# Kernel tuning notes

Hardware: AMD Instinct MI355X
Metric: run time of the kernel (lower is better)

## Reference

```python
import jax, jax.numpy as jnp
import numpy as np

N = 20000      # nodes
E = 320000     # edges (before self-loops)
G = 64         # graphs in batch
IN = 128       # in_channels
HID = 64       # hidden_dim
NEG_SLOPE = 0.2


def setup_inputs() -> dict:
    key = jax.random.key(0)
    ks = jax.random.split(key, 20)
    def glorot(k, shape):
        fan = shape[0] + shape[-1]
        return jax.random.normal(k, shape, jnp.float32) * np.sqrt(2.0 / fan)
    inp = {
        'x': jax.random.normal(ks[0], (N, IN), jnp.float32),
        'edge_index': jax.random.randint(ks[1], (2, E), 0, N, jnp.int32),
        'batch': jnp.sort(jax.random.randint(ks[2], (N,), 0, G, jnp.int32)),
        # GAT layer 1: heads=4, out=64, concat=False
        'W1': glorot(ks[3], (IN, 4 * HID)),
        'as1': glorot(ks[4], (4, HID)),
        'ad1': glorot(ks[5], (4, HID)),
        'b1': jnp.zeros((HID,), jnp.float32),
        # GAT layer 2: heads=2, out=32, concat=False
        'W2': glorot(ks[6], (HID, 2 * (HID // 2))),
        'as2': glorot(ks[7], (2, HID // 2)),
        'ad2': glorot(ks[8], (2, HID // 2)),
        'b2': jnp.zeros((HID // 2,), jnp.float32),
        # continue head: 32->16->1
        'cW1': glorot(ks[9], (HID // 2, HID // 4)), 'cb1': jnp.zeros((HID // 4,), jnp.float32),
        'cW2': glorot(ks[10], (HID // 4, 1)), 'cb2': jnp.zeros((1,), jnp.float32),
        # halt head: 32->16->1
        'hW1': glorot(ks[11], (HID // 2, HID // 4)), 'hb1': jnp.zeros((HID // 4,), jnp.float32),
        'hW2': glorot(ks[12], (HID // 4, 1)), 'hb2': jnp.zeros((1,), jnp.float32),
    }
    return inp


def gat_layer(x, src, dst, W, att_src, att_dst, bias, heads, out_ch):
    # x: [N, Fin] -> h: [N, H, C]
    n = x.shape[0]
    h = (x @ W).reshape(n, heads, out_ch)
    a_src = jnp.einsum('nhc,hc->nh', h, att_src)   # [N, H]
    a_dst = jnp.einsum('nhc,hc->nh', h, att_dst)   # [N, H]
    e = jax.nn.leaky_relu(a_src[src] + a_dst[dst], NEG_SLOPE)   # [E', H]
    # segment softmax over incoming edges of each dst node
    m = jax.ops.segment_max(e, dst, num_segments=n)             # [N, H]
    ee = jnp.exp(e - m[dst])
    denom = jax.ops.segment_sum(ee, dst, num_segments=n)        # [N, H]
    alpha = ee / (denom[dst] + 1e-16)                           # [E', H]
    msg = h[src] * alpha[:, :, None]                            # [E', H, C]
    out = jax.ops.segment_sum(msg, dst, num_segments=n)         # [N, H, C]
    return out.mean(axis=1) + bias                              # concat=False -> head mean


def reference(x, edge_index, batch, W1, as1, ad1, b1, W2, as2, ad2, b2,
              cW1, cb1, cW2, cb2, hW1, hb1, hW2, hb2):
    n = x.shape[0]
    loop = jnp.arange(n, dtype=edge_index.dtype)
    src = jnp.concatenate([edge_index[0], loop])   # add self-loops (PyG default)
    dst = jnp.concatenate([edge_index[1], loop])

    h1 = jax.nn.relu(gat_layer(x, src, dst, W1, as1, ad1, b1, 4, HID))
    h2 = jax.nn.relu(gat_layer(h1, src, dst, W2, as2, ad2, b2, 2, HID // 2))

    # global mean pool per graph
    sums = jax.ops.segment_sum(h2, batch, num_segments=G)                 # [G, 32]
    cnt = jax.ops.segment_sum(jnp.ones((n,), h2.dtype), batch, num_segments=G)
    emb = sums / jnp.maximum(cnt, 1.0)[:, None]                           # [G, 32]

    cont = jax.nn.sigmoid(jax.nn.relu(emb @ cW1 + cb1) @ cW2 + cb2)       # [G, 1]
    halt = jax.nn.sigmoid(jax.nn.relu(emb @ hW1 + hb1) @ hW2 + hb2)       # [G, 1]
    return (halt, cont)
```

## Files before the change

### kernel.cpp

```cpp
#include <hip/hip_runtime.h>
#include <hip/hip_fp16.h>


#define G_GRAPHS 64

using half8   = __attribute__((ext_vector_type(8))) _Float16;
using half4v  = __attribute__((ext_vector_type(4))) _Float16;
using floatx4 = __attribute__((ext_vector_type(4))) float;
using floatx2 = __attribute__((ext_vector_type(2))) float;

__global__ __launch_bounds__(256) void init_deg_ell(
        int4* __restrict__ deg4, int* __restrict__ col_ell, int N)
{
    int i = blockIdx.x * 256 + threadIdx.x;
    int n4 = N * 4;
    if (i < n4) {
        deg4[i] = ((i & 3) == 0) ? int4{1, 0, 0, 0} : int4{0, 0, 0, 0};
        if ((i & 3) == 0) {
            int n = i >> 2;
            col_ell[(size_t)n * 64] = n;
        }
    }
}

__global__ __launch_bounds__(256) void ell_gemm1(
        const int* __restrict__ ei, int* __restrict__ deg16,
        int* __restrict__ col_ell, int E0, int mb,
        const float* __restrict__ A, const float* __restrict__ B,
        unsigned char* __restrict__ C8, const float* __restrict__ att_s,
        const float* __restrict__ att_d, float* __restrict__ a_s,
        float* __restrict__ a_d, int M)
{
    __shared__ _Float16 As[64][136];
    __shared__ _Float16 Bt[64][136];

    if ((int)blockIdx.x >= mb) {
        int idx4 = ((int)blockIdx.x - mb) * 1024 + threadIdx.x * 4;
        if (idx4 + 3 < E0) {
            int4 s4 = *reinterpret_cast<const int4*>(&ei[idx4]);
            int4 d4 = *reinterpret_cast<const int4*>(&ei[E0 + idx4]);
            int sl0 = atomicAdd(&deg16[d4.x << 4], 1);
            int sl1 = atomicAdd(&deg16[d4.y << 4], 1);
            int sl2 = atomicAdd(&deg16[d4.z << 4], 1);
            int sl3 = atomicAdd(&deg16[d4.w << 4], 1);
            if (sl0 < 64) col_ell[(size_t)d4.x * 64 + sl0] = s4.x;
            if (sl1 < 64) col_ell[(size_t)d4.y * 64 + sl1] = s4.y;
            if (sl2 < 64) col_ell[(size_t)d4.z * 64 + sl2] = s4.z;
            if (sl3 < 64) col_ell[(size_t)d4.w * 64 + sl3] = s4.w;
        } else {
            for (int j = 0; j < 4; j++) {
                int idx = idx4 + j;
                if (idx < E0) {
                    int src = ei[idx];
                    int dst = ei[E0 + idx];
                    int slot = atomicAdd(&deg16[dst << 4], 1);
                    if (slot < 64)
                        col_ell[(size_t)dst * 64 + slot] = src;
                }
            }
        }
        return;
    }

    const int tid  = threadIdx.x;
    const int row0 = blockIdx.x * 64;
    const int wid  = tid >> 6;
    const int lane = tid & 63;
    const int r    = lane & 15;
    const int quad = lane >> 4;
    const int rw0  = wid * 16;

    const int arow = tid >> 2;
    const int akc  = (tid & 3) * 32;
    const int agr  = row0 + arow;

    #pragma unroll
    for (int i = 0; i < 4; i++) {
        half8 v = {};
        if (agr < M) {
            const float* p = &A[(size_t)agr * 128 + akc + i * 8];
            float4 f0 = *reinterpret_cast<const float4*>(p);
            float4 f1 = *reinterpret_cast<const float4*>(p + 4);
            v[0] = (_Float16)f0.x; v[1] = (_Float16)f0.y;
            v[2] = (_Float16)f0.z; v[3] = (_Float16)f0.w;
            v[4] = (_Float16)f1.x; v[5] = (_Float16)f1.y;
            v[6] = (_Float16)f1.z; v[7] = (_Float16)f1.w;
        }
        *reinterpret_cast<half8*>(&As[arow][akc + i * 8]) = v;
    }

    for (int by = 0; by < 4; by++) {
        __syncthreads();

        #pragma unroll
        for (int i = 0; i < 8; i++) {
            int id = tid + 256 * i;
            int k  = id >> 4;
            int n4 = (id & 15) * 4;
            float4 f = *reinterpret_cast<const float4*>(
                &B[(size_t)k * 256 + by * 64 + n4]);
            Bt[n4 + 0][k] = (_Float16)f.x;
            Bt[n4 + 1][k] = (_Float16)f.y;
            Bt[n4 + 2][k] = (_Float16)f.z;
            Bt[n4 + 3][k] = (_Float16)f.w;
        }
        __syncthreads();

        floatx4 acc[4] = {};
        #pragma unroll
        for (int s = 0; s < 4; s++) {
            half8 af = *reinterpret_cast<const half8*>(&As[rw0 + r][s * 32 + quad * 8]);
            #pragma unroll
            for (int nt = 0; nt < 4; nt++) {
                half8 bf = *reinterpret_cast<const half8*>(&Bt[nt * 16 + r][s * 32 + quad * 8]);
                acc[nt] = __builtin_amdgcn_mfma_f32_16x16x32_f16(af, bf, acc[nt], 0, 0, 0);
            }
        }

        float ps[4], pd[4];
        #pragma unroll
        for (int reg = 0; reg < 4; reg++) { ps[reg] = 0.f; pd[reg] = 0.f; }
        #pragma unroll
        for (int nt = 0; nt < 4; nt++) {
            int cl = nt * 16 + r;
            float ws = att_s[by * 64 + cl];
            float wd = att_d[by * 64 + cl];
            #pragma unroll
            for (int reg = 0; reg < 4; reg++) {
                ps[reg] += acc[nt][reg] * ws;
                pd[reg] += acc[nt][reg] * wd;
            }
        }
        #pragma unroll
        for (int off = 1; off < 16; off <<= 1)
            #pragma unroll
            for (int reg = 0; reg < 4; reg++) {
                ps[reg] += __shfl_xor(ps[reg], off);
                pd[reg] += __shfl_xor(pd[reg], off);
            }
        if (r == 0) {
            #pragma unroll
            for (int reg = 0; reg < 4; reg++) {
                int gr = row0 + rw0 + quad * 4 + reg;
                if (gr < M) {
                    a_s[gr * 4 + by] = ps[reg];
                    a_d[gr * 4 + by] = pd[reg];
                }
            }
        }

        __syncthreads();
        unsigned char (*lds8)[80] = reinterpret_cast<unsigned char(*)[80]>(&Bt[0][0]);
        #pragma unroll
        for (int nt = 0; nt < 4; nt++) {
            #pragma unroll
            for (int reg = 0; reg < 4; reg++) {
                int wv = __builtin_amdgcn_cvt_pk_fp8_f32(
                    acc[nt][reg], acc[nt][reg], 0, false);
                lds8[rw0 + quad * 4 + reg][nt * 16 + r] = (unsigned char)(wv & 0xFF);
            }
        }
        __syncthreads();
        {
            int row = tid >> 2;
            int c16 = (tid & 3) * 16;
            int gr  = row0 + row;
            if (gr < M) {
                int4 v = *reinterpret_cast<const int4*>(&lds8[row][c16]);
                *reinterpret_cast<int4*>(&C8[(size_t)gr * 256 + by * 64 + c16]) = v;
            }
        }
    }
}

__global__ __launch_bounds__(256) void gemm2_kernel(
        const _Float16* __restrict__ A, const float* __restrict__ B,
        unsigned char* __restrict__ C8, const float* __restrict__ att_s,
        const float* __restrict__ att_d, float* __restrict__ a_s,
        float* __restrict__ a_d, int M)
{
    __shared__ _Float16 As[64][72];
    __shared__ _Float16 Bt[64][72];

    const int tid  = threadIdx.x;
    const int row0 = blockIdx.x * 64;

    {
        int row = tid >> 2;
        int kc  = (tid & 3) * 16;
        int gr  = row0 + row;
        #pragma unroll
        for (int i = 0; i < 2; i++) {
            half8 v = {};
            if (gr < M)
                v = *reinterpret_cast<const half8*>(&A[(size_t)gr * 64 + kc + i * 8]);
            *reinterpret_cast<half8*>(&As[row][kc + i * 8]) = v;
        }
    }
    {
        #pragma unroll
        for (int i = 0; i < 4; i++) {
            int id = tid + 256 * i;
            int k  = id >> 4;
            int n4 = (id & 15) * 4;
            float4 f = *reinterpret_cast<const float4*>(&B[(size_t)k * 64 + n4]);
            Bt[n4 + 0][k] = (_Float16)f.x;
            Bt[n4 + 1][k] = (_Float16)f.y;
            Bt[n4 + 2][k] = (_Float16)f.z;
            Bt[n4 + 3][k] = (_Float16)f.w;
        }
    }
    __syncthreads();

    const int wid  = tid >> 6;
    const int lane = tid & 63;
    const int r    = lane & 15;
    const int quad = lane >> 4;
    const int rw0  = wid * 16;

    floatx4 acc[4] = {};
    #pragma unroll
    for (int s = 0; s < 2; s++) {
        half8 af = *reinterpret_cast<const half8*>(&As[rw0 + r][s * 32 + quad * 8]);
        #pragma unroll
        for (int nt = 0; nt < 4; nt++) {
            half8 bf = *reinterpret_cast<const half8*>(&Bt[nt * 16 + r][s * 32 + quad * 8]);
            acc[nt] = __builtin_amdgcn_mfma_f32_16x16x32_f16(af, bf, acc[nt], 0, 0, 0);
        }
    }

    float ps[2][4], pd[2][4];
    #pragma unroll
    for (int hl = 0; hl < 2; hl++)
        #pragma unroll
        for (int reg = 0; reg < 4; reg++) { ps[hl][reg] = 0.f; pd[hl][reg] = 0.f; }
    #pragma unroll
    for (int nt = 0; nt < 4; nt++) {
        int hl = nt >> 1;
        int cl = (nt & 1) * 16 + r;
        float ws = att_s[hl * 32 + cl];
        float wd = att_d[hl * 32 + cl];
        #pragma unroll
        for (int reg = 0; reg < 4; reg++) {
            ps[hl][reg] += acc[nt][reg] * ws;
            pd[hl][reg] += acc[nt][reg] * wd;
        }
    }
    #pragma unroll
    for (int off = 1; off < 16; off <<= 1)
        #pragma unroll
        for (int hl = 0; hl < 2; hl++)
            #pragma unroll
            for (int reg = 0; reg < 4; reg++) {
                ps[hl][reg] += __shfl_xor(ps[hl][reg], off);
                pd[hl][reg] += __shfl_xor(pd[hl][reg], off);
            }
    if (r == 0) {
        #pragma unroll
        for (int reg = 0; reg < 4; reg++) {
            int gr = row0 + rw0 + quad * 4 + reg;
            if (gr < M) {
                #pragma unroll
                for (int hl = 0; hl < 2; hl++) {
                    a_s[gr * 2 + hl] = ps[hl][reg];
                    a_d[gr * 2 + hl] = pd[hl][reg];
                }
            }
        }
    }

    __syncthreads();
    unsigned char (*lds8)[80] = reinterpret_cast<unsigned char(*)[80]>(&As[0][0]);
    #pragma unroll
    for (int nt = 0; nt < 4; nt++) {
        #pragma unroll
        for (int reg = 0; reg < 4; reg++) {
            int wv = __builtin_amdgcn_cvt_pk_fp8_f32(
                acc[nt][reg], acc[nt][reg], 0, false);
            lds8[rw0 + quad * 4 + reg][nt * 16 + r] = (unsigned char)(wv & 0xFF);
        }
    }
    __syncthreads();
    {
        int row = tid >> 2;
        int c16 = (tid & 3) * 16;
        int gr  = row0 + row;
        if (gr < M) {
            int4 v = *reinterpret_cast<const int4*>(&lds8[row][c16]);
            *reinterpret_cast<int4*>(&C8[(size_t)gr * 64 + c16]) = v;
        }
    }
}

__device__ inline void facc4_h(float* a, float2 raw, float p) {
    __half2 h0 = *reinterpret_cast<__half2*>(&raw.x);
    __half2 h1 = *reinterpret_cast<__half2*>(&raw.y);
    float2 f0 = __half22float2(h0), f1 = __half22float2(h1);
    a[0] += p * f0.x; a[1] += p * f0.y; a[2] += p * f1.x; a[3] += p * f1.y;
}
__device__ inline void facc4_8(float* a, unsigned int w, float p) {
    floatx2 lo = __builtin_amdgcn_cvt_pk_f32_fp8((int)w, false);
    floatx2 hi = __builtin_amdgcn_cvt_pk_f32_fp8((int)w, true);
    a[0] += p * lo[0]; a[1] += p * lo[1]; a[2] += p * hi[0]; a[3] += p * hi[1];
}
__device__ inline void facc8_8(float* a, uint2 w, float p) {
    facc4_8(a,     w.x, p);
    facc4_8(a + 4, w.y, p);
}
__device__ inline float fp8_dec1(unsigned char b) {
    floatx2 lo = __builtin_amdgcn_cvt_pk_f32_fp8((int)(unsigned int)b, false);
    return lo[0];
}

template<int H, int C, bool OUT_HALF, bool FEAT_FP8>
__device__ void gat_general(
        int d, int lo, int degc, const int* __restrict__ colidx,
        const void* __restrict__ hfeat_v, const float* __restrict__ a_s,
        const float* __restrict__ a_d, const float* __restrict__ bias,
        void* __restrict__ out_v, int N, float* p_wave)
{
    if (d >= N) return;
    constexpr int FV = (H * C) / 64;
    const int lane = threadIdx.x & 63;
    const int hi = lo + degc;
    const __half* hfeat = (const __half*)hfeat_v;
    const unsigned char* ffeat = (const unsigned char*)hfeat_v;
    const int h_lane = (lane * FV) / C;

    float adp[H];
    #pragma unroll
    for (int h = 0; h < H; h++) adp[h] = a_d[d * H + h];
    float lh[H];
    #pragma unroll
    for (int h = 0; h < H; h++) lh[h] = 0.f;
    float acc[FV];
    #pragma unroll
    for (int v = 0; v < FV; v++) acc[v] = 0.f;

    float mh[H];
    #pragma unroll
    for (int h = 0; h < H; h++) mh[h] = -3.0e38f;
    for (int i = lo + lane; i < hi; i += 64) {
        int s = colidx[i];
        #pragma unroll
        for (int h = 0; h < H; h++) {
            float v = a_s[s * H + h] + adp[h];
            v = (v > 0.f) ? v : 0.2f * v;
            mh[h] = fmaxf(mh[h], v);
        }
    }
    #pragma unroll
    for (int off = 1; off < 64; off <<= 1)
        #pragma unroll
        for (int h = 0; h < H; h++)
            mh[h] = fmaxf(mh[h], __shfl_xor(mh[h], off));

    for (int base = lo; base < hi; base += 64) {
        int i = base + lane;
        int s = 0;
        if (i < hi) {
            s = colidx[i];
            #pragma unroll
            for (int h = 0; h < H; h++) {
                float v = a_s[s * H + h] + adp[h];
                v = (v > 0.f) ? v : 0.2f * v;
                float p = __expf(v - mh[h]);
                lh[h] += p;
                p_wave[(i - base) * H + h] = p;
            }
        }
        int cnt = min(64, hi - base);
        for (int j = 0; j < cnt; j++) {
            int s_j = __shfl(s, j);
            float pj = p_wave[j * H + h_lane];
            if constexpr (FV == 4 && FEAT_FP8) {
                unsigned int raw = *reinterpret_cast<const unsigned int*>(
                    ffeat + (size_t)s_j * (H * C) + lane * 4);
                facc4_8(acc, raw, pj);
            } else if constexpr (FV == 4) {
                float2 raw = *reinterpret_cast<const float2*>(
                    hfeat + (size_t)s_j * (H * C) + lane * 4);
                facc4_h(acc, raw, pj);
            } else if constexpr (FEAT_FP8) {
                acc[0] += pj * fp8_dec1(ffeat[(size_t)s_j * (H * C) + lane]);
            } else {
                acc[0] += pj * __half2float(hfeat[(size_t)s_j * (H * C) + lane]);
            }
        }
    }
    #pragma unroll
    for (int off = 1; off < 64; off <<= 1)
        #pragma unroll
        for (int h = 0; h < H; h++)
            lh[h] += __shfl_xor(lh[h], off);

    float lsel = lh[0];
    #pragma unroll
    for (int h = 1; h < H; h++) if (h_lane == h) lsel = lh[h];
    const float inv = 1.0f / (lsel + 1e-16f);

    if constexpr (FV == 4) {
        float vx = acc[0] * inv, vy = acc[1] * inv,
              vz = acc[2] * inv, vw = acc[3] * inv;
        vx += __shfl_xor(vx, 16); vy += __shfl_xor(vy, 16);
        vz += __shfl_xor(vz, 16); vw += __shfl_xor(vw, 16);
        vx += __shfl_xor(vx, 32); vy += __shfl_xor(vy, 32);
        vz += __shfl_xor(vz, 32); vw += __shfl_xor(vw, 32);
        if (lane < 16) {
            float4 bv = *reinterpret_cast<const float4*>(&bias[lane * 4]);
            float ox = fmaxf(0.25f * vx + bv.x, 0.f);
            float oy = fmaxf(0.25f * vy + bv.y, 0.f);
            float oz = fmaxf(0.25f * vz + bv.z, 0.f);
            float ow = fmaxf(0.25f * vw + bv.w, 0.f);
            if constexpr (OUT_HALF) {
                half4v hv = { (_Float16)ox, (_Float16)oy, (_Float16)oz, (_Float16)ow };
                *reinterpret_cast<half4v*>((_Float16*)out_v + (size_t)d * C + lane * 4) = hv;
            } else {
                float4 o = make_float4(ox, oy, oz, ow);
                *reinterpret_cast<float4*>((float*)out_v + (size_t)d * C + lane * 4) = o;
            }
        }
    } else {
        float v = acc[0] * inv;
        v += __shfl_xor(v, 32);
        if (lane < 32) {
            float o = fmaxf(0.5f * v + bias[lane], 0.f);
            if constexpr (OUT_HALF)
                ((_Float16*)out_v)[(size_t)d * C + lane] = (_Float16)o;
            else
                ((float*)out_v)[(size_t)d * C + lane] = o;
        }
    }
}

template<int H, int C, bool OUT_HALF, bool FEAT_FP8>
__global__ __launch_bounds__(256) void gat_dst(
        const int* __restrict__ degv, const int* __restrict__ col_ell,
        const void* __restrict__ hfeat_v, const float* __restrict__ a_s,
        const float* __restrict__ a_d, const float* __restrict__ bias,
        void* __restrict__ out_v, int N)
{
    const int wid  = threadIdx.x >> 6;
    const int lane = threadIdx.x & 63;
    const int nw   = lane >> 5;
    const int l32  = lane & 31;

    __shared__ float p_sh[4][64 * H];

    const int d  = blockIdx.x * 8 + wid * 2 + nw;
    const bool nodeok = (d < N);
    const int lo = d * 64;

    int degc = 0;
    if (nodeok) degc = min(degv[d << 4], 64);
    const int degA = __shfl(degc, 0);
    const int degB = __shfl(degc, 32);
    const bool fast = (degA <= 32) && (degB <= 32);

    if (fast) {
        const __half* hfeat = (const __half*)hfeat_v;
        const unsigned char* ffeat = (const unsigned char*)hfeat_v;

        float adp[H];
        #pragma unroll
        for (int h = 0; h < H; h++) adp[h] = nodeok ? a_d[d * H + h] : 0.f;

        int s = 0;
        float lh[H];
        #pragma unroll
        for (int h = 0; h < H; h++) lh[h] = 0.f;
        const bool valid = nodeok && (l32 < degc);
        if (valid) {
            s = col_ell[lo + l32];
            if constexpr (H == 4) {
                float4 av = *reinterpret_cast<const float4*>(&a_s[s * 4]);
                float ev[4] = {av.x + adp[0], av.y + adp[1],
                               av.z + adp[2], av.w + adp[3]};
                #pragma unroll
                for (int h = 0; h < 4; h++) {
                    float e = (ev[h] > 0.f) ? ev[h] : 0.2f * ev[h];
                    float p = __expf(e);
                    lh[h] = p;
                    p_sh[wid][nw * 32 * H + l32 * H + h] = p;
                }
            } else {
                float2 av = *reinterpret_cast<const float2*>(&a_s[s * 2]);
                float ev[2] = {av.x + adp[0], av.y + adp[1]};
                #pragma unroll
                for (int h = 0; h < 2; h++) {
                    float e = (ev[h] > 0.f) ? ev[h] : 0.2f * ev[h];
                    float p = __expf(e);
                    lh[h] = p;
                    p_sh[wid][nw * 32 * H + l32 * H + h] = p;
                }
            }
        }
        #pragma unroll
        for (int off = 1; off < 32; off <<= 1)
            #pragma unroll
            for (int h = 0; h < H; h++)
                lh[h] += __shfl_xor(lh[h], off);

        const int sbase = nw * 32;

        if constexpr (H == 4) {
            const int hl = l32 >> 3;
            float a0[8] = {}, a1[8] = {};
            int j = 0;
            for (; j + 8 <= degc; j += 8) {
                uint2 raw[8]; float pw[8];
                #pragma unroll
                for (int u = 0; u < 8; u++) {
                    int sj = __shfl(s, sbase + j + u);
                    pw[u]  = p_sh[wid][nw * 128 + (j + u) * 4 + hl];
                    raw[u] = *reinterpret_cast<const uint2*>(
                        ffeat + (size_t)sj * 256 + l32 * 8);
                }
                #pragma unroll
                for (int u = 0; u < 8; u++)
                    facc8_8((u & 1) ? a1 : a0, raw[u], pw[u]);
            }
            for (; j < degc; j++) {
                int sj = __shfl(s, sbase + j);
                float pw = p_sh[wid][nw * 128 + j * 4 + hl];
                uint2 raw = *reinterpret_cast<const uint2*>(
                    ffeat + (size_t)sj * 256 + l32 * 8);
                facc8_8(a0, raw, pw);
            }
            #pragma unroll
            for (int k = 0; k < 8; k++) a0[k] += a1[k];

            float lsel = lh[0];
            #pragma unroll
            for (int h = 1; h < 4; h++) if (hl == h) lsel = lh[h];
            float inv = 1.0f / (lsel + 1e-16f);
            #pragma unroll
            for (int k = 0; k < 8; k++) {
                float v = a0[k] * inv;
                v += __shfl_xor(v, 8);
                v += __shfl_xor(v, 16);
                a0[k] = v;
            }
            if (nodeok && l32 < 8) {
                float4 b0 = *reinterpret_cast<const float4*>(&bias[l32 * 8]);
                float4 b1 = *reinterpret_cast<const float4*>(&bias[l32 * 8 + 4]);
                float bb[8] = {b0.x, b0.y, b0.z, b0.w, b1.x, b1.y, b1.z, b1.w};
                half8 hv;
                #pragma unroll
                for (int k = 0; k < 8; k++)
                    hv[k] = (_Float16)fmaxf(0.25f * a0[k] + bb[k], 0.f);
                *reinterpret_cast<half8*>((_Float16*)out_v + (size_t)d * 64 + l32 * 8) = hv;
            }
        } else {
            const int q   = l32 >> 4;
            const int l16 = l32 & 15;
            const int hl2 = l16 >> 3;
            float a0[4] = {}, a1[4] = {};
            int j = 0;
            for (; j + 8 <= degc; j += 8) {
                unsigned int raw[4]; float pw[4];
                #pragma unroll
                for (int u = 0; u < 4; u++) {
                    int je = j + 2 * u + q;
                    int sj = __shfl(s, sbase + je);
                    pw[u]  = p_sh[wid][nw * 64 + je * 2 + hl2];
                    raw[u] = *reinterpret_cast<const unsigned int*>(
                        ffeat + (size_t)sj * 64 + l16 * 4);
                }
                #pragma unroll
                for (int u = 0; u < 4; u++)
                    facc4_8((u & 1) ? a1 : a0, raw[u], pw[u]);
            }
            for (int jr = j + q; jr < degc; jr += 2) {
                int sj = __shfl(s, sbase + jr);
                float pw = p_sh[wid][nw * 64 + jr * 2 + hl2];
                unsigned int raw = *reinterpret_cast<const unsigned int*>(
                    ffeat + (size_t)sj * 64 + l16 * 4);
                facc4_8(a0, raw, pw);
            }
            #pragma unroll
            for (int k = 0; k < 4; k++) {
                a0[k] += a1[k];
                a0[k] += __shfl_xor(a0[k], 16);
            }
            float lsel = (hl2 == 0) ? lh[0] : lh[1];
            float inv = 1.0f / (lsel + 1e-16f);
            #pragma unroll
            for (int k = 0; k < 4; k++) {
                float v = a0[k] * inv;
                v += __shfl_xor(v, 8);
                a0[k] = v;
            }
            if (nodeok && l32 < 8) {
                float4 bb = *reinterpret_cast<const float4*>(&bias[l32 * 4]);
                float4 o;
                o.x = fmaxf(0.5f * a0[0] + bb.x, 0.f);
                o.y = fmaxf(0.5f * a0[1] + bb.y, 0.f);
                o.z = fmaxf(0.5f * a0[2] + bb.z, 0.f);
                o.w = fmaxf(0.5f * a0[3] + bb.w, 0.f);
                *reinterpret_cast<float4*>((float*)out_v + (size_t)d * 32 + l32 * 4) = o;
            }
        }
        return;
    }

    const int dA = blockIdx.x * 8 + wid * 2;
    gat_general<H, C, OUT_HALF, FEAT_FP8>(
        dA, dA * 64, __shfl(degc, 0), col_ell,
        hfeat_v, a_s, a_d, bias, out_v, N, p_sh[wid]);
    gat_general<H, C, OUT_HALF, FEAT_FP8>(
        dA + 1, (dA + 1) * 64, __shfl(degc, 32), col_ell,
        hfeat_v, a_s, a_d, bias, out_v, N, p_sh[wid]);
}

__global__ __launch_bounds__(256) void pool_heads(
        const float* __restrict__ h2, const int* __restrict__ batch,
        const float* __restrict__ cW1, const float* __restrict__ cb1,
        const float* __restrict__ cW2, const float* __restrict__ cb2,
        const float* __restrict__ hW1, const float* __restrict__ hb1,
        const float* __restrict__ hW2, const float* __restrict__ hb2,
        float* __restrict__ out, int N)
{
    const int g = blockIdx.x;
    const int c = threadIdx.x & 31;
    const int r = threadIdx.x >> 5;

    __shared__ int bounds[2];
    __shared__ float red[8][32];
    __shared__ float emb_s[32];
    __shared__ float hidden[32];

    if (threadIdx.x < 2) {
        int target = g + (int)threadIdx.x;
        int lo = 0, hi = N;
        while (lo < hi) {
            int mid = (lo + hi) >> 1;
            if (batch[mid] < target) lo = mid + 1; else hi = mid;
        }
        bounds[threadIdx.x] = lo;
    }
    __syncthreads();
    const int lo = bounds[0], hi = bounds[1];

    float acc = 0.f;
    for (int n = lo + r; n < hi; n += 8)
        acc += h2[(size_t)n * 32 + c];
    red[r][c] = acc;
    __syncthreads();
    if (r == 0) {
        float s = 0.f;
        #pragma unroll
        for (int i = 0; i < 8; i++) s += red[i][c];
        emb_s[c] = s / fmaxf((float)(hi - lo), 1.0f);
    }
    __syncthreads();

    if (threadIdx.x < 32) {
        int j = threadIdx.x & 15;
        bool is_halt = threadIdx.x >= 16;
        const float* w1v = is_halt ? hW1 : cW1;
        const float* b1v = is_halt ? hb1 : cb1;
        const float* w2v = is_halt ? hW2 : cW2;
        float s = b1v[j];
        #pragma unroll
        for (int cc = 0; cc < 32; cc++) s += emb_s[cc] * w1v[cc * 16 + j];
        hidden[threadIdx.x] = fmaxf(s, 0.f) * w2v[j];
    }
    __syncthreads();
    if (threadIdx.x == 0) {
        float sc = cb2[0], sh = hb2[0];
        #pragma unroll
        for (int i = 0; i < 16; i++) { sc += hidden[i]; sh += hidden[16 + i]; }
        out[g]            = 1.0f / (1.0f + __expf(-sh));
        out[G_GRAPHS + g] = 1.0f / (1.0f + __expf(-sc));
    }
}

extern "C" void kernel_launch(void* const* d_in, const int* in_sizes, int n_in,
                              void* d_out, int out_size, void* d_ws, size_t ws_size,
                              hipStream_t stream)
{
    const float* x   = (const float*)d_in[0];
    const int*   ei  = (const int*)  d_in[1];
    const int*   bat = (const int*)  d_in[2];
    const float* W1  = (const float*)d_in[3];
    const float* as1 = (const float*)d_in[4];
    const float* ad1 = (const float*)d_in[5];
    const float* b1  = (const float*)d_in[6];
    const float* W2  = (const float*)d_in[7];
    const float* as2 = (const float*)d_in[8];
    const float* ad2 = (const float*)d_in[9];
    const float* b2  = (const float*)d_in[10];
    const float* cW1 = (const float*)d_in[11];
    const float* cb1 = (const float*)d_in[12];
    const float* cW2 = (const float*)d_in[13];
    const float* cb2 = (const float*)d_in[14];
    const float* hW1 = (const float*)d_in[15];
    const float* hb1 = (const float*)d_in[16];
    const float* hW2 = (const float*)d_in[17];
    const float* hb2 = (const float*)d_in[18];

    const int N    = in_sizes[2];
    const int E0   = in_sizes[1] / 2;

    float* w = (float*)d_ws;
    size_t o = 0;
    unsigned char* h1pre_f8 = (unsigned char*)(w + o); o += (size_t)N * 64;
    _Float16* h1_h    = (_Float16*)(w + o); o += (size_t)N * 32;
    unsigned char* h2pre_f8 = (unsigned char*)(w + o); o += (size_t)N * 16;
    float* a_s1  = w + o; o += (size_t)N * 4;
    float* a_d1  = w + o; o += (size_t)N * 4;
    float* a_s2  = w + o; o += (size_t)N * 2;
    float* a_d2  = w + o; o += (size_t)N * 2;
    float* h2    = w + o; o += (size_t)N * 32;
    int* deg16   = (int*)(w + o); o += (size_t)N * 16;
    int* col_ell = (int*)(w + o); o += (size_t)N * 64;
    (void)ws_size; (void)n_in; (void)out_size;

    const dim3 blk(256);
    const int eb4 = (E0 + 1023) / 1024;
    const int nb8 = (N + 7) / 8;
    const int mb  = (N + 63) / 64;

    const int n4 = N * 4;
    init_deg_ell<<<(n4 + 255) / 256, blk, 0, stream>>>(
        (int4*)deg16, col_ell, N);

    ell_gemm1<<<mb + eb4, blk, 0, stream>>>(
        ei, deg16, col_ell, E0, mb,
        x, W1, h1pre_f8, as1, ad1, a_s1, a_d1, N);

    gat_dst<4, 64, true, true><<<nb8, blk, 0, stream>>>(
        deg16, col_ell, h1pre_f8, a_s1, a_d1, b1, h1_h, N);

    gemm2_kernel<<<mb, blk, 0, stream>>>(
        h1_h, W2, h2pre_f8, as2, ad2, a_s2, a_d2, N);
    gat_dst<2, 32, false, true><<<nb8, blk, 0, stream>>>(
        deg16, col_ell, h2pre_f8, a_s2, a_d2, b2, h2, N);

    pool_heads<<<G_GRAPHS, blk, 0, stream>>>(
        h2, bat, cW1, cb1, cW2, cb2, hW1, hb1, hW2, hb2, (float*)d_out, N);
}
```

Baseline: 102.5 us.

## Build ELL adjacency per node-range block with LDS counters, drop init kernel

New measurement: 250.8 us. 145% more time.

```diff
diff --git a/kernel.cpp b/kernel.cpp
--- a/kernel.cpp
+++ b/kernel.cpp
@@ -3,29 +3,16 @@
 
 
 #define G_GRAPHS 64
+#define NPB 160
 
 using half8   = __attribute__((ext_vector_type(8))) _Float16;
 using half4v  = __attribute__((ext_vector_type(4))) _Float16;
 using floatx4 = __attribute__((ext_vector_type(4))) float;
 using floatx2 = __attribute__((ext_vector_type(2))) float;
 
-__global__ __launch_bounds__(256) void init_deg_ell(
-        int4* __restrict__ deg4, int* __restrict__ col_ell, int N)
-{
-    int i = blockIdx.x * 256 + threadIdx.x;
-    int n4 = N * 4;
-    if (i < n4) {
-        deg4[i] = ((i & 3) == 0) ? int4{1, 0, 0, 0} : int4{0, 0, 0, 0};
-        if ((i & 3) == 0) {
-            int n = i >> 2;
-            col_ell[(size_t)n * 64] = n;
-        }
-    }
-}
-
 __global__ __launch_bounds__(256) void ell_gemm1(
-        const int* __restrict__ ei, int* __restrict__ deg16,
-        int* __restrict__ col_ell, int E0, int mb,
+        const int* __restrict__ ei, int* __restrict__ deg,
+        int* __restrict__ col_ell, int E0, int mb, int N,
         const float* __restrict__ A, const float* __restrict__ B,
         unsigned char* __restrict__ C8, const float* __restrict__ att_s,
         const float* __restrict__ att_d, float* __restrict__ a_s,
@@ -34,35 +21,63 @@
     __shared__ _Float16 As[64][136];
     __shared__ _Float16 Bt[64][136];
 
+    const int tid = threadIdx.x;
+
     if ((int)blockIdx.x >= mb) {
-        int idx4 = ((int)blockIdx.x - mb) * 1024 + threadIdx.x * 4;
-        if (idx4 + 3 < E0) {
-            int4 s4 = *reinterpret_cast<const int4*>(&ei[idx4]);
-            int4 d4 = *reinterpret_cast<const int4*>(&ei[E0 + idx4]);
-            int sl0 = atomicAdd(&deg16[d4.x << 4], 1);
-            int sl1 = atomicAdd(&deg16[d4.y << 4], 1);
-            int sl2 = atomicAdd(&deg16[d4.z << 4], 1);
-            int sl3 = atomicAdd(&deg16[d4.w << 4], 1);
-            if (sl0 < 64) col_ell[(size_t)d4.x * 64 + sl0] = s4.x;
-            if (sl1 < 64) col_ell[(size_t)d4.y * 64 + sl1] = s4.y;
-            if (sl2 < 64) col_ell[(size_t)d4.z * 64 + sl2] = s4.z;
-            if (sl3 < 64) col_ell[(size_t)d4.w * 64 + sl3] = s4.w;
-        } else {
-            for (int j = 0; j < 4; j++) {
-                int idx = idx4 + j;
-                if (idx < E0) {
-                    int src = ei[idx];
-                    int dst = ei[E0 + idx];
-                    int slot = atomicAdd(&deg16[dst << 4], 1);
-                    if (slot < 64)
-                        col_ell[(size_t)dst * 64 + slot] = src;
-                }
-            }
-        }
+        int* lcnt = reinterpret_cast<int*>(&As[0][0]);
+        const int base = ((int)blockIdx.x - mb) * NPB;
+        const int cnt  = min(NPB, N - base);
+        if (cnt <= 0) return;
+
+        for (int i = tid; i < cnt; i += 256) {
+            lcnt[i] = 1;
+            col_ell[(size_t)(base + i) * 64] = base + i;
+        }
+        __syncthreads();
+
+        const int* __restrict__ dstp = ei + E0;
+        for (int idx = tid * 4; idx + 3 < E0; idx += 1024) {
+            int4 d4 = *reinterpret_cast<const int4*>(&dstp[idx]);
+            unsigned r0 = (unsigned)(d4.x - base);
+            unsigned r1 = (unsigned)(d4.y - base);
+            unsigned r2 = (unsigned)(d4.z - base);
+            unsigned r3 = (unsigned)(d4.w - base);
+            if (r0 < (unsigned)cnt) {
+                int slot = atomicAdd(&lcnt[r0], 1);
+                if (slot < 64)
+                    col_ell[(size_t)(base + (int)r0) * 64 + slot] = ei[idx];
+            }
+            if (r1 < (unsigned)cnt) {
+                int slot = atomicAdd(&lcnt[r1], 1);
+                if (slot < 64)
+                    col_ell[(size_t)(base + (int)r1) * 64 + slot] = ei[idx + 1];
+            }
+            if (r2 < (unsigned)cnt) {
+                int slot = atomicAdd(&lcnt[r2], 1);
+                if (slot < 64)
+                    col_ell[(size_t)(base + (int)r2) * 64 + slot] = ei[idx + 2];
+            }
+            if (r3 < (unsigned)cnt) {
+                int slot = atomicAdd(&lcnt[r3], 1);
+                if (slot < 64)
+                    col_ell[(size_t)(base + (int)r3) * 64 + slot] = ei[idx + 3];
+            }
+        }
+        for (int idx = (E0 & ~3) + tid; idx < E0; idx += 256) {
+            int dst = dstp[idx];
+            unsigned r = (unsigned)(dst - base);
+            if (r < (unsigned)cnt) {
+                int slot = atomicAdd(&lcnt[r], 1);
+                if (slot < 64)
+                    col_ell[(size_t)dst * 64 + slot] = ei[idx];
+            }
+        }
+        __syncthreads();
+        for (int i = tid; i < cnt; i += 256)
+            deg[base + i] = lcnt[i];
         return;
     }
 
-    const int tid  = threadIdx.x;
     const int row0 = blockIdx.x * 64;
     const int wid  = tid >> 6;
     const int lane = tid & 63;
@@ -452,7 +467,7 @@
     const int lo = d * 64;
 
     int degc = 0;
-    if (nodeok) degc = min(degv[d << 4], 64);
+    if (nodeok) degc = min(degv[d], 64);
     const int degA = __shfl(degc, 0);
     const int degB = __shfl(degc, 32);
     const bool fast = (degA <= 32) && (degB <= 32);
@@ -713,30 +728,26 @@
     float* a_s2  = w + o; o += (size_t)N * 2;
     float* a_d2  = w + o; o += (size_t)N * 2;
     float* h2    = w + o; o += (size_t)N * 32;
-    int* deg16   = (int*)(w + o); o += (size_t)N * 16;
+    int* deg     = (int*)(w + o); o += (size_t)N;
     int* col_ell = (int*)(w + o); o += (size_t)N * 64;
     (void)ws_size; (void)n_in; (void)out_size;
 
     const dim3 blk(256);
-    const int eb4 = (E0 + 1023) / 1024;
+    const int pb  = (N + NPB - 1) / NPB;
     const int nb8 = (N + 7) / 8;
     const int mb  = (N + 63) / 64;
 
-    const int n4 = N * 4;
-    init_deg_ell<<<(n4 + 255) / 256, blk, 0, stream>>>(
-        (int4*)deg16, col_ell, N);
-
-    ell_gemm1<<<mb + eb4, blk, 0, stream>>>(
-        ei, deg16, col_ell, E0, mb,
+    ell_gemm1<<<mb + pb, blk, 0, stream>>>(
+        ei, deg, col_ell, E0, mb, N,
         x, W1, h1pre_f8, as1, ad1, a_s1, a_d1, N);
 
     gat_dst<4, 64, true, true><<<nb8, blk, 0, stream>>>(
-        deg16, col_ell, h1pre_f8, a_s1, a_d1, b1, h1_h, N);
+        deg, col_ell, h1pre_f8, a_s1, a_d1, b1, h1_h, N);
 
     gemm2_kernel<<<mb, blk, 0, stream>>>(
         h1_h, W2, h2pre_f8, as2, ad2, a_s2, a_d2, N);
     gat_dst<2, 32, false, true><<<nb8, blk, 0, stream>>>(
-        deg16, col_ell, h2pre_f8, a_s2, a_d2, b2, h2, N);
+        deg, col_ell, h2pre_f8, a_s2, a_d2, b2, h2, N);
 
     pool_heads<<<G_GRAPHS, blk, 0, stream>>>(
         h2, bat, cW1, cb1, cW2, cb2, hW1, hb1, hW2, hb2, (float*)d_out, N);
```
